# Performance work log

Measured on AMD Instinct MI355X. Metric: run time of the kernel, lower is better.

The kernel has to match this reference:

```python
import jax, jax.numpy as jnp
import numpy as np

OUT = 7            # output_size
SR = 2             # sampling_ratio (samples per bin per axis)
SCALES = (0.25, 0.125, 0.0625, 0.03125)
CANON_SIZE = 224.0
CANON_LVL = 4.0
MIN_LVL = 2
IMG = 800.0


def setup_inputs() -> dict:
    key = jax.random.key(0)
    kf = jax.random.split(key, 6)
    B, C, R = 2, 256, 256
    sizes = [200, 100, 50, 25]
    feats = [jax.random.normal(kf[i], (B, C, s, s), jnp.float32) for i, s in enumerate(sizes)]
    # valid xyxy boxes in [0, IMG], log-uniform side lengths -> spread across FPN levels
    ctr = jax.random.uniform(kf[4], (B, R, 2), minval=0.0, maxval=IMG)
    wh = jnp.exp(jax.random.uniform(kf[5], (B, R, 2), minval=float(np.log(16.0)), maxval=float(np.log(512.0))))
    lo = jnp.clip(ctr - wh / 2, 0.0, IMG)
    hi = jnp.clip(ctr + wh / 2, 0.0, IMG)
    boxes = jnp.concatenate([lo, hi], axis=-1)  # [B,R,4]
    return {"feat0": feats[0], "feat1": feats[1], "feat2": feats[2], "feat3": feats[3], "boxes": boxes}


def _prep(c, lim):
    """torchvision ROIAlign (aligned=False) bilinear index prep.
    c: sample coords [N,OUT,SR]; lim: per-box feature extent (H or W) [N]."""
    limb = lim[:, None, None]
    valid = (c > -1.0) & (c < limb)          # out-of-range samples contribute 0
    cc = jnp.maximum(c, 0.0)
    low = jnp.floor(cc)
    cap = limb - 1.0
    at_edge = low >= cap                      # y_low >= H-1 -> clamp, frac = 0
    low = jnp.minimum(low, cap)
    high = jnp.minimum(low + 1.0, cap)
    cc = jnp.where(at_edge, low, cc)
    frac = cc - low
    return valid, low.astype(jnp.int32), high.astype(jnp.int32), frac


def roi_pooler(feats, boxes):
    B, R = boxes.shape[0], boxes.shape[1]
    C = feats[0].shape[1]
    N = B * R
    flat = boxes.reshape(N, 4)
    bidx = jnp.repeat(jnp.arange(B, dtype=jnp.int32), R)  # batch index per ROI

    # level assignment (assign_boxes_to_levels)
    area = (flat[:, 2] - flat[:, 0]) * (flat[:, 3] - flat[:, 1])
    lvl = jnp.floor(CANON_LVL + jnp.log2(jnp.sqrt(area) / CANON_SIZE + 1e-8))
    lvl = jnp.clip(lvl, MIN_LVL, MIN_LVL + len(feats) - 1).astype(jnp.int32) - MIN_LVL  # [N] in [0,3]

    # pad all levels to P2 size and stack so each ROI is sampled once at its level
    Hm, Wm = feats[0].shape[2], feats[0].shape[3]
    padded = jnp.stack([jnp.pad(f, ((0, 0), (0, 0), (0, Hm - f.shape[2]), (0, Wm - f.shape[3]))) for f in feats])
    fp = padded.transpose(0, 1, 3, 4, 2)  # [L,B,Hm,Wm,C] channels-last for gather
    Hs = jnp.array([f.shape[2] for f in feats], jnp.float32)[lvl]
    Ws = jnp.array([f.shape[3] for f in feats], jnp.float32)[lvl]
    scale = jnp.array(SCALES, jnp.float32)[lvl]

    # ROIAlign aligned=False: scale coords, clamp roi size to >= 1
    x1 = flat[:, 0] * scale
    y1 = flat[:, 1] * scale
    x2 = flat[:, 2] * scale
    y2 = flat[:, 3] * scale
    roi_w = jnp.maximum(x2 - x1, 1.0)
    roi_h = jnp.maximum(y2 - y1, 1.0)
    bw = roi_w / OUT
    bh = roi_h / OUT

    # sample grid: bin index + sub-sample offsets -> [N,OUT,SR]
    grid = jnp.arange(OUT, dtype=jnp.float32)[None, :, None] + (jnp.arange(SR, dtype=jnp.float32)[None, None, :] + 0.5) / SR
    ys = y1[:, None, None] + bh[:, None, None] * grid
    xs = x1[:, None, None] + bw[:, None, None] * grid

    vy, yl, yh, fy = _prep(ys, Hs)
    vx, xl, xh, fx = _prep(xs, Ws)

    P = OUT * OUT * SR * SR  # all sample points per ROI

    def by(a):  # y-axis quantity -> broadcast over (out_y,out_x,sr_y,sr_x)
        return jnp.broadcast_to(a[:, :, None, :, None], (N, OUT, OUT, SR, SR)).reshape(N, P)

    def bx(a):
        return jnp.broadcast_to(a[:, None, :, None, :], (N, OUT, OUT, SR, SR)).reshape(N, P)

    YL, YH, FY, VY = by(yl), by(yh), by(fy), by(vy)
    XL, XH, FX, VX = bx(xl), bx(xh), bx(fx), bx(vx)

    li = lvl[:, None]
    bi = bidx[:, None]
    v00 = fp[li, bi, YL, XL]  # [N,P,C]
    v01 = fp[li, bi, YL, XH]
    v10 = fp[li, bi, YH, XL]
    v11 = fp[li, bi, YH, XH]

    w = lambda a: a[..., None]
    val = (w((1 - FY) * (1 - FX)) * v00 + w((1 - FY) * FX) * v01
           + w(FY * (1 - FX)) * v10 + w(FY * FX) * v11)
    val = val * w((VY & VX).astype(val.dtype))
    out = val.reshape(N, OUT, OUT, SR * SR, C).mean(axis=3)  # average over SR*SR samples
    return out.transpose(0, 3, 1, 2)  # [N,C,OUT,OUT]


def reference(feat0, feat1, feat2, feat3, boxes):
    return roi_pooler([feat0, feat1, feat2, feat3], boxes)
```

## Files before the change

### kernel.cpp

```cpp
#include <hip/hip_runtime.h>
#include <math.h>

typedef unsigned short u16;
typedef unsigned int   u32;

#define OUTSZ 7
#define B_ 2
#define C_ 256
#define R_ 256
#define N_ (B_ * R_)

#define PX_TOTAL 106250
#define WS_INFO_OFF 0
#define WS_NHWC_OFF (512 * 1024)
#define WS_NEEDED (WS_NHWC_OFF + (size_t)PX_TOTAL * 256 * 2)

struct RoiInfo2 {
    int pxBase, W;
    float wy0[14], wy1[14], wx0[14], wx1[14];
    short yl[14], yh[14], xl[14], xh[14];
};

__device__ __forceinline__ u16 f2bf(float v) {
    u32 u = __float_as_uint(v);
    u += 0x7fffu + ((u >> 16) & 1u);
    return (u16)(u >> 16);
}

__device__ __forceinline__ u32 pack2bf(float a, float b) {
    return (u32)f2bf(a) | ((u32)f2bf(b) << 16);
}

__global__ __launch_bounds__(256) void roi_prep(const float* __restrict__ boxes,
                                                RoiInfo2* __restrict__ info)
{
    int n = blockIdx.x * 256 + threadIdx.x;
    if (n >= N_) return;

    const float* bx = boxes + (size_t)n * 4;
    float x1 = bx[0], y1 = bx[1], x2 = bx[2], y2 = bx[3];
    float area = (x2 - x1) * (y2 - y1);
    float lf = floorf(4.0f + log2f(sqrtf(area) / 224.0f + 1e-8f));
    lf = fminf(fmaxf(lf, 2.0f), 5.0f);
    int lvl = (int)lf - 2;

    const float scales[4] = {0.25f, 0.125f, 0.0625f, 0.03125f};
    const int   sizes[4]  = {200, 100, 50, 25};
    const int   bases[4]  = {0, 80000, 100000, 105000};
    float scale = scales[lvl];
    int   HW    = sizes[lvl];
    int   b     = n >> 8;

    float fx1 = x1 * scale, fy1 = y1 * scale;
    float roi_w = fmaxf(x2 * scale - fx1, 1.0f);
    float roi_h = fmaxf(y2 * scale - fy1, 1.0f);
    float bw = roi_w / (float)OUTSZ;
    float bh = roi_h / (float)OUTSZ;

    RoiInfo2 ri;
    ri.W = HW;
    ri.pxBase = bases[lvl] + b * HW * HW;

    float lim = (float)HW, cap = lim - 1.0f;
    #pragma unroll
    for (int i = 0; i < 14; ++i) {
        float g = (float)(i >> 1) + ((float)(i & 1) + 0.5f) * 0.5f;
        {
            float c = fy1 + bh * g;
            bool  v = (c > -1.0f) && (c < lim);
            float cc = fmaxf(c, 0.0f);
            float low = floorf(cc);
            bool  edge = low >= cap;
            low = fminf(low, cap);
            float high = fminf(low + 1.0f, cap);
            float fr = edge ? 0.0f : (cc - low);
            ri.yl[i] = (short)(int)low;
            ri.yh[i] = (short)(int)high;
            ri.wy0[i] = v ? (1.0f - fr) : 0.0f;
            ri.wy1[i] = v ? fr : 0.0f;
        }
        {
            float c = fx1 + bw * g;
            bool  v = (c > -1.0f) && (c < lim);
            float cc = fmaxf(c, 0.0f);
            float low = floorf(cc);
            bool  edge = low >= cap;
            low = fminf(low, cap);
            float high = fminf(low + 1.0f, cap);
            float fr = edge ? 0.0f : (cc - low);
            ri.xl[i] = (short)(int)low;
            ri.xh[i] = (short)(int)high;
            ri.wx0[i] = v ? (1.0f - fr) : 0.0f;
            ri.wx1[i] = v ? fr : 0.0f;
        }
    }
    info[n] = ri;
}

__global__ __launch_bounds__(256) void nhwc_cast(
    const float* __restrict__ f0, const float* __restrict__ f1,
    const float* __restrict__ f2, const float* __restrict__ f3,
    u16* __restrict__ dst)
{
    __shared__ u32 lds32[256 * 32];
    const int tid  = threadIdx.x;
    const int lane = tid & 63;
    const int wave = tid >> 6;

    const int t  = blockIdx.x;
    const int cb = blockIdx.y;
    const int b  = blockIdx.z;
    const float* src; int HWsz, dstBase, ft;
    if      (t < 157) { src = f0; HWsz = 40000; dstBase = 0;      ft = t;       }
    else if (t < 197) { src = f1; HWsz = 10000; dstBase = 80000;  ft = t - 157; }
    else if (t < 207) { src = f2; HWsz = 2500;  dstBase = 100000; ft = t - 197; }
    else              { src = f3; HWsz = 625;   dstBase = 105000; ft = t - 207; }

    const int fbase = ft * 256;
    const int cw    = cb * 64 + wave * 16;
    const int rem   = HWsz - fbase;
    const int p0    = 4 * lane;
    const bool vec  = ((HWsz & 3) == 0) && (p0 + 3 < rem);

    const float* base = src + ((size_t)(b * C_ + cw)) * HWsz + fbase;

    float f[16][4];
    #pragma unroll
    for (int i = 0; i < 16; ++i) {
        const float* row = base + (size_t)i * HWsz;
        if (vec) {
            float4 v = *(const float4*)(row + p0);
            f[i][0] = v.x; f[i][1] = v.y; f[i][2] = v.z; f[i][3] = v.w;
        } else {
            #pragma unroll
            for (int k = 0; k < 4; ++k)
                f[i][k] = (p0 + k < rem) ? row[p0 + k] : 0.0f;
        }
    }

    #pragma unroll
    for (int r = 0; r < 2; ++r) {
        #pragma unroll
        for (int j = 0; j < 4; ++j) {
            uint4 o;
            o.x = pack2bf(f[r * 8 + 0][j], f[r * 8 + 1][j]);
            o.y = pack2bf(f[r * 8 + 2][j], f[r * 8 + 3][j]);
            o.z = pack2bf(f[r * 8 + 4][j], f[r * 8 + 5][j]);
            o.w = pack2bf(f[r * 8 + 6][j], f[r * 8 + 7][j]);
            const int q = (wave * 2 + r) ^ (lane & 7);
            *(uint4*)&lds32[(p0 + j) * 32 + q * 4] = o;
        }
    }
    __syncthreads();

    const int maxpx = rem < 256 ? rem : 256;
    #pragma unroll
    for (int i = 0; i < 8; ++i) {
        const int idx = i * 256 + tid;
        const int px  = idx >> 3;
        const int sub = idx & 7;
        if (px < maxpx) {
            const int q = sub ^ ((px >> 2) & 7);
            uint4 o = *(const uint4*)&lds32[px * 32 + q * 4];
            *(uint4*)(dst + (size_t)(dstBase + b * HWsz + fbase + px) * 256 + cb * 64 + sub * 8) = o;
        }
    }
}

__global__ __launch_bounds__(256) void roi_gather(
    const u16* __restrict__ ws16, const RoiInfo2* __restrict__ info,
    float* __restrict__ out)
{
    __shared__ float lds[128 * 49];
    const int g    = blockIdx.x;
    const int n    = blockIdx.y;
    const int tid  = threadIdx.x;
    const int lane = tid & 63;
    const int wave = tid >> 6;
    const RoiInfo2& ri = info[n];
    const int W = ri.W, base = ri.pxBase;
    const int c0 = g * 128;

    for (int cell = wave; cell < 49; cell += 4) {
        const int cu = __builtin_amdgcn_readfirstlane(cell);
        const int oy = cu / 7, ox = cu - oy * 7;
        float a0 = 0.0f, a1 = 0.0f;
        #pragma unroll
        for (int sy = 0; sy < 2; ++sy) {
            const int ei = oy * 2 + sy;
            const float wy0 = ri.wy0[ei], wy1 = ri.wy1[ei];
            const int rl = base + ri.yl[ei] * W;
            const int rh = base + ri.yh[ei] * W;
            #pragma unroll
            for (int sx = 0; sx < 2; ++sx) {
                const int ej = ox * 2 + sx;
                const float w00 = wy0 * ri.wx0[ej], w01 = wy0 * ri.wx1[ej];
                const float w10 = wy1 * ri.wx0[ej], w11 = wy1 * ri.wx1[ej];
                const int xl = ri.xl[ej], xh = ri.xh[ej];
                u32 u00 = ((const u32*)(ws16 + (size_t)(rl + xl) * 256 + c0))[lane];
                u32 u01 = ((const u32*)(ws16 + (size_t)(rl + xh) * 256 + c0))[lane];
                u32 u10 = ((const u32*)(ws16 + (size_t)(rh + xl) * 256 + c0))[lane];
                u32 u11 = ((const u32*)(ws16 + (size_t)(rh + xh) * 256 + c0))[lane];
                a0 += w00 * __uint_as_float(u00 << 16) + w01 * __uint_as_float(u01 << 16)
                    + w10 * __uint_as_float(u10 << 16) + w11 * __uint_as_float(u11 << 16);
                a1 += w00 * __uint_as_float(u00 & 0xffff0000u) + w01 * __uint_as_float(u01 & 0xffff0000u)
                    + w10 * __uint_as_float(u10 & 0xffff0000u) + w11 * __uint_as_float(u11 & 0xffff0000u);
            }
        }
        lds[(2 * lane) * 49 + cu]     = a0 * 0.25f;
        lds[(2 * lane + 1) * 49 + cu] = a1 * 0.25f;
    }
    __syncthreads();

    const float4* lv = (const float4*)lds;
    float4* ov = (float4*)(out + ((size_t)(n * C_ + c0)) * 49);
    for (int i = tid; i < 1568; i += 256) ov[i] = lv[i];
}

__global__ __launch_bounds__(256) void roi_direct(
    const float* __restrict__ f0, const float* __restrict__ f1,
    const float* __restrict__ f2, const float* __restrict__ f3,
    const float* __restrict__ boxes, float* __restrict__ out)
{
    const int total = B_ * R_ * C_ * OUTSZ * OUTSZ;
    int idx = blockIdx.x * blockDim.x + threadIdx.x;
    if (idx >= total) return;
    int ox = idx % 7, oy = (idx / 7) % 7, c = (idx / 49) % C_, n = idx / (49 * C_), b = n >> 8;
    const float* bx = boxes + (size_t)n * 4;
    float x1 = bx[0], y1 = bx[1], x2 = bx[2], y2 = bx[3];
    float lf = floorf(4.0f + log2f(sqrtf((x2 - x1) * (y2 - y1)) / 224.0f + 1e-8f));
    int lvl = (int)fminf(fmaxf(lf, 2.0f), 5.0f) - 2;
    const float scales[4] = {0.25f, 0.125f, 0.0625f, 0.03125f};
    const int sizes[4] = {200, 100, 50, 25};
    float scale = scales[lvl]; int HW = sizes[lvl];
    const float* fl = lvl == 0 ? f0 : lvl == 1 ? f1 : lvl == 2 ? f2 : f3;
    float fx1 = x1 * scale, fy1 = y1 * scale;
    float bw = fmaxf(x2 * scale - fx1, 1.0f) / 7.0f, bh = fmaxf(y2 * scale - fy1, 1.0f) / 7.0f;
    const float* plane = fl + ((size_t)(b * C_ + c)) * HW * HW;
    float lim = (float)HW, cap = lim - 1.0f, acc = 0.0f;
    #pragma unroll
    for (int sy = 0; sy < 2; sy++) {
        float yc = fy1 + bh * ((float)oy + ((float)sy + 0.5f) * 0.5f);
        bool vy = (yc > -1.0f) && (yc < lim);
        float ccy = fmaxf(yc, 0.0f), lowy = floorf(ccy);
        bool ey = lowy >= cap; lowy = fminf(lowy, cap);
        float highy = fminf(lowy + 1.0f, cap);
        float wfy = ey ? 0.0f : (ccy - lowy);
        int yl = (int)lowy, yh = (int)highy;
        #pragma unroll
        for (int sx = 0; sx < 2; sx++) {
            float xc = fx1 + bw * ((float)ox + ((float)sx + 0.5f) * 0.5f);
            bool vx = (xc > -1.0f) && (xc < lim);
            float ccx = fmaxf(xc, 0.0f), lowx = floorf(ccx);
            bool ex = lowx >= cap; lowx = fminf(lowx, cap);
            float highx = fminf(lowx + 1.0f, cap);
            float wfx = ex ? 0.0f : (ccx - lowx);
            int xl = (int)lowx, xh = (int)highx;
            if (vy && vx) {
                float v00 = plane[yl * HW + xl], v01 = plane[yl * HW + xh];
                float v10 = plane[yh * HW + xl], v11 = plane[yh * HW + xh];
                acc += (1.0f - wfy) * ((1.0f - wfx) * v00 + wfx * v01)
                     + wfy * ((1.0f - wfx) * v10 + wfx * v11);
            }
        }
    }
    out[idx] = acc * 0.25f;
}

extern "C" void kernel_launch(void* const* d_in, const int* in_sizes, int n_in,
                              void* d_out, int out_size, void* d_ws, size_t ws_size,
                              hipStream_t stream) {
    const float* f0    = (const float*)d_in[0];
    const float* f1    = (const float*)d_in[1];
    const float* f2    = (const float*)d_in[2];
    const float* f3    = (const float*)d_in[3];
    const float* boxes = (const float*)d_in[4];
    float* out = (float*)d_out;

    if (ws_size < WS_NEEDED) {
        const int total = B_ * R_ * C_ * OUTSZ * OUTSZ;
        roi_direct<<<(total + 255) / 256, 256, 0, stream>>>(f0, f1, f2, f3, boxes, out);
        return;
    }

    RoiInfo2* info = (RoiInfo2*)((char*)d_ws + WS_INFO_OFF);
    u16*      nhwc = (u16*)((char*)d_ws + WS_NHWC_OFF);

    roi_prep<<<dim3(2), 256, 0, stream>>>(boxes, info);
    nhwc_cast<<<dim3(210, 4, 2), 256, 0, stream>>>(f0, f1, f2, f3, nhwc);
    roi_gather<<<dim3(2, N_), 256, 0, stream>>>(nhwc, info, out);
}
```

Measured before the change: 189.7 us.

## Fold ROI prep into gather, split gather by cells, halve cast LDS

Removes the separate roi_prep kernel launch: each gather block now computes its ROI's sampling indices and weights into shared memory. The gather blocks are split over output cells instead of channels, so each lane reads 4 contiguous bf16 channels (uint2) and writes through a padded LDS tile with nontemporal stores. The nhwc_cast kernel halves its LDS footprint by staging in two passes and raises occupancy via launch bounds, and uses nontemporal loads. This trades extra per-block prep work and a scattered output store pattern for one fewer launch and higher cast occupancy.

```diff
diff --git a/kernel.cpp b/kernel.cpp
--- a/kernel.cpp
+++ b/kernel.cpp
@@ -3,6 +3,7 @@
 
 typedef unsigned short u16;
 typedef unsigned int   u32;
+typedef float f32x4 __attribute__((ext_vector_type(4)));
 
 #define OUTSZ 7
 #define B_ 2
@@ -11,15 +12,7 @@
 #define N_ (B_ * R_)
 
 #define PX_TOTAL 106250
-#define WS_INFO_OFF 0
-#define WS_NHWC_OFF (512 * 1024)
-#define WS_NEEDED (WS_NHWC_OFF + (size_t)PX_TOTAL * 256 * 2)
-
-struct RoiInfo2 {
-    int pxBase, W;
-    float wy0[14], wy1[14], wx0[14], wx1[14];
-    short yl[14], yh[14], xl[14], xh[14];
-};
+#define WS_NEEDED ((size_t)PX_TOTAL * 256 * 2)
 
 __device__ __forceinline__ u16 f2bf(float v) {
     u32 u = __float_as_uint(v);
@@ -31,78 +24,12 @@
     return (u32)f2bf(a) | ((u32)f2bf(b) << 16);
 }
 
-__global__ __launch_bounds__(256) void roi_prep(const float* __restrict__ boxes,
-                                                RoiInfo2* __restrict__ info)
-{
-    int n = blockIdx.x * 256 + threadIdx.x;
-    if (n >= N_) return;
-
-    const float* bx = boxes + (size_t)n * 4;
-    float x1 = bx[0], y1 = bx[1], x2 = bx[2], y2 = bx[3];
-    float area = (x2 - x1) * (y2 - y1);
-    float lf = floorf(4.0f + log2f(sqrtf(area) / 224.0f + 1e-8f));
-    lf = fminf(fmaxf(lf, 2.0f), 5.0f);
-    int lvl = (int)lf - 2;
-
-    const float scales[4] = {0.25f, 0.125f, 0.0625f, 0.03125f};
-    const int   sizes[4]  = {200, 100, 50, 25};
-    const int   bases[4]  = {0, 80000, 100000, 105000};
-    float scale = scales[lvl];
-    int   HW    = sizes[lvl];
-    int   b     = n >> 8;
-
-    float fx1 = x1 * scale, fy1 = y1 * scale;
-    float roi_w = fmaxf(x2 * scale - fx1, 1.0f);
-    float roi_h = fmaxf(y2 * scale - fy1, 1.0f);
-    float bw = roi_w / (float)OUTSZ;
-    float bh = roi_h / (float)OUTSZ;
-
-    RoiInfo2 ri;
-    ri.W = HW;
-    ri.pxBase = bases[lvl] + b * HW * HW;
-
-    float lim = (float)HW, cap = lim - 1.0f;
-    #pragma unroll
-    for (int i = 0; i < 14; ++i) {
-        float g = (float)(i >> 1) + ((float)(i & 1) + 0.5f) * 0.5f;
-        {
-            float c = fy1 + bh * g;
-            bool  v = (c > -1.0f) && (c < lim);
-            float cc = fmaxf(c, 0.0f);
-            float low = floorf(cc);
-            bool  edge = low >= cap;
-            low = fminf(low, cap);
-            float high = fminf(low + 1.0f, cap);
-            float fr = edge ? 0.0f : (cc - low);
-            ri.yl[i] = (short)(int)low;
-            ri.yh[i] = (short)(int)high;
-            ri.wy0[i] = v ? (1.0f - fr) : 0.0f;
-            ri.wy1[i] = v ? fr : 0.0f;
-        }
-        {
-            float c = fx1 + bw * g;
-            bool  v = (c > -1.0f) && (c < lim);
-            float cc = fmaxf(c, 0.0f);
-            float low = floorf(cc);
-            bool  edge = low >= cap;
-            low = fminf(low, cap);
-            float high = fminf(low + 1.0f, cap);
-            float fr = edge ? 0.0f : (cc - low);
-            ri.xl[i] = (short)(int)low;
-            ri.xh[i] = (short)(int)high;
-            ri.wx0[i] = v ? (1.0f - fr) : 0.0f;
-            ri.wx1[i] = v ? fr : 0.0f;
-        }
-    }
-    info[n] = ri;
-}
-
-__global__ __launch_bounds__(256) void nhwc_cast(
+__global__ __launch_bounds__(256, 8) void nhwc_cast(
     const float* __restrict__ f0, const float* __restrict__ f1,
     const float* __restrict__ f2, const float* __restrict__ f3,
     u16* __restrict__ dst)
 {
-    __shared__ u32 lds32[256 * 32];
+    __shared__ u32 lds32[128 * 32];
     const int tid  = threadIdx.x;
     const int lane = tid & 63;
     const int wave = tid >> 6;
@@ -129,7 +56,7 @@
     for (int i = 0; i < 16; ++i) {
         const float* row = base + (size_t)i * HWsz;
         if (vec) {
-            float4 v = *(const float4*)(row + p0);
+            f32x4 v = __builtin_nontemporal_load((const f32x4*)(row + p0));
             f[i][0] = v.x; f[i][1] = v.y; f[i][2] = v.z; f[i][3] = v.w;
         } else {
             #pragma unroll
@@ -138,83 +65,153 @@
         }
     }
 
+    const int half  = lane >> 5;
+    const int pl0   = p0 & 127;
+    const int maxpx = rem < 256 ? rem : 256;
+
     #pragma unroll
-    for (int r = 0; r < 2; ++r) {
+    for (int h = 0; h < 2; ++h) {
+        if (half == h) {
+            #pragma unroll
+            for (int r = 0; r < 2; ++r) {
+                #pragma unroll
+                for (int j = 0; j < 4; ++j) {
+                    uint4 o;
+                    o.x = pack2bf(f[r * 8 + 0][j], f[r * 8 + 1][j]);
+                    o.y = pack2bf(f[r * 8 + 2][j], f[r * 8 + 3][j]);
+                    o.z = pack2bf(f[r * 8 + 4][j], f[r * 8 + 5][j]);
+                    o.w = pack2bf(f[r * 8 + 6][j], f[r * 8 + 7][j]);
+                    const int q = (wave * 2 + r) ^ (lane & 7);
+                    *(uint4*)&lds32[(pl0 + j) * 32 + q * 4] = o;
+                }
+            }
+        }
+        __syncthreads();
+
         #pragma unroll
-        for (int j = 0; j < 4; ++j) {
-            uint4 o;
-            o.x = pack2bf(f[r * 8 + 0][j], f[r * 8 + 1][j]);
-            o.y = pack2bf(f[r * 8 + 2][j], f[r * 8 + 3][j]);
-            o.z = pack2bf(f[r * 8 + 4][j], f[r * 8 + 5][j]);
-            o.w = pack2bf(f[r * 8 + 6][j], f[r * 8 + 7][j]);
-            const int q = (wave * 2 + r) ^ (lane & 7);
-            *(uint4*)&lds32[(p0 + j) * 32 + q * 4] = o;
-        }
-    }
-    __syncthreads();
-
-    const int maxpx = rem < 256 ? rem : 256;
-    #pragma unroll
-    for (int i = 0; i < 8; ++i) {
-        const int idx = i * 256 + tid;
-        const int px  = idx >> 3;
-        const int sub = idx & 7;
-        if (px < maxpx) {
-            const int q = sub ^ ((px >> 2) & 7);
-            uint4 o = *(const uint4*)&lds32[px * 32 + q * 4];
-            *(uint4*)(dst + (size_t)(dstBase + b * HWsz + fbase + px) * 256 + cb * 64 + sub * 8) = o;
-        }
+        for (int i = 0; i < 4; ++i) {
+            const int idx = i * 256 + tid;
+            const int pxl = idx >> 3;
+            const int sub = idx & 7;
+            const int px  = h * 128 + pxl;
+            if (px < maxpx) {
+                const int q = sub ^ ((pxl >> 2) & 7);
+                uint4 o = *(const uint4*)&lds32[pxl * 32 + q * 4];
+                *(uint4*)(dst + (size_t)(dstBase + b * HWsz + fbase + px) * 256 + cb * 64 + sub * 8) = o;
+            }
+        }
+        if (h == 0) __syncthreads();
+    }
+}
+
+__device__ __forceinline__ void acc4(float4& a, uint2 u, float w) {
+    a.x += w * __uint_as_float(u.x << 16);
+    a.y += w * __uint_as_float(u.x & 0xffff0000u);
+    a.z += w * __uint_as_float(u.y << 16);
+    a.w += w * __uint_as_float(u.y & 0xffff0000u);
+}
+
+template<int NC, int CB>
+__device__ __forceinline__ void store_out(const float* lds, float* out, int n) {
+    #pragma unroll 4
+    for (int i = threadIdx.x; i < 256 * NC; i += 256) {
+        const int c = i / NC;
+        const int j = i - c * NC;
+        __builtin_nontemporal_store(lds[j * 260 + c],
+                                    out + ((size_t)(n * C_ + c)) * 49 + CB + j);
     }
 }
 
 __global__ __launch_bounds__(256) void roi_gather(
-    const u16* __restrict__ ws16, const RoiInfo2* __restrict__ info,
+    const u16* __restrict__ ws16, const float* __restrict__ boxes,
     float* __restrict__ out)
 {
-    __shared__ float lds[128 * 49];
+    __shared__ float lds[28 * 260];
+    __shared__ float s_wy0[14], s_wy1[14], s_wx0[14], s_wx1[14];
+    __shared__ int   s_yl[14], s_yh[14], s_xl[14], s_xh[14];
+    __shared__ int   s_base, s_W;
+
     const int g    = blockIdx.x;
     const int n    = blockIdx.y;
     const int tid  = threadIdx.x;
     const int lane = tid & 63;
     const int wave = tid >> 6;
-    const RoiInfo2& ri = info[n];
-    const int W = ri.W, base = ri.pxBase;
-    const int c0 = g * 128;
-
-    for (int cell = wave; cell < 49; cell += 4) {
+
+    if (tid < 28) {
+        const float* bx = boxes + (size_t)n * 4;
+        float x1 = bx[0], y1 = bx[1], x2 = bx[2], y2 = bx[3];
+        float area = (x2 - x1) * (y2 - y1);
+        float lf = floorf(4.0f + log2f(sqrtf(area) / 224.0f + 1e-8f));
+        lf = fminf(fmaxf(lf, 2.0f), 5.0f);
+        int lvl = (int)lf - 2;
+        const float scales[4] = {0.25f, 0.125f, 0.0625f, 0.03125f};
+        const int   sizes[4]  = {200, 100, 50, 25};
+        const int   bases[4]  = {0, 80000, 100000, 105000};
+        float scale = scales[lvl];
+        int   HW    = sizes[lvl];
+        float lim = (float)HW, cap = lim - 1.0f;
+        float fx1 = x1 * scale, fy1 = y1 * scale;
+        float bw = fmaxf(x2 * scale - fx1, 1.0f) / (float)OUTSZ;
+        float bh = fmaxf(y2 * scale - fy1, 1.0f) / (float)OUTSZ;
+        if (tid == 0) { s_base = bases[lvl] + (n >> 8) * HW * HW; s_W = HW; }
+
+        const int  i   = (tid < 14) ? tid : tid - 14;
+        const bool isy = tid < 14;
+        float o  = isy ? fy1 : fx1;
+        float st = isy ? bh  : bw;
+        float gq = (float)(i >> 1) + ((float)(i & 1) + 0.5f) * 0.5f;
+        float c = o + st * gq;
+        bool  v = (c > -1.0f) && (c < lim);
+        float cc = fmaxf(c, 0.0f);
+        float low = floorf(cc);
+        bool  edge = low >= cap;
+        low = fminf(low, cap);
+        float high = fminf(low + 1.0f, cap);
+        float fr = edge ? 0.0f : (cc - low);
+        float w0 = v ? (1.0f - fr) : 0.0f;
+        float w1 = v ? fr : 0.0f;
+        if (isy) { s_yl[i] = (int)low; s_yh[i] = (int)high; s_wy0[i] = w0; s_wy1[i] = w1; }
+        else     { s_xl[i] = (int)low; s_xh[i] = (int)high; s_wx0[i] = w0; s_wx1[i] = w1; }
+    }
+    __syncthreads();
+
+    const int base = s_base, W = s_W;
+    const int CB = g ? 28 : 0;
+    const int NC = g ? 21 : 28;
+
+    for (int cell = CB + wave; cell < CB + NC; cell += 4) {
         const int cu = __builtin_amdgcn_readfirstlane(cell);
         const int oy = cu / 7, ox = cu - oy * 7;
-        float a0 = 0.0f, a1 = 0.0f;
+        float4 acc = {0.0f, 0.0f, 0.0f, 0.0f};
         #pragma unroll
         for (int sy = 0; sy < 2; ++sy) {
             const int ei = oy * 2 + sy;
-            const float wy0 = ri.wy0[ei], wy1 = ri.wy1[ei];
-            const int rl = base + ri.yl[ei] * W;
-            const int rh = base + ri.yh[ei] * W;
+            const float wy0 = s_wy0[ei], wy1 = s_wy1[ei];
+            const int rl = base + s_yl[ei] * W;
+            const int rh = base + s_yh[ei] * W;
             #pragma unroll
             for (int sx = 0; sx < 2; ++sx) {
                 const int ej = ox * 2 + sx;
-                const float w00 = wy0 * ri.wx0[ej], w01 = wy0 * ri.wx1[ej];
-                const float w10 = wy1 * ri.wx0[ej], w11 = wy1 * ri.wx1[ej];
-                const int xl = ri.xl[ej], xh = ri.xh[ej];
-                u32 u00 = ((const u32*)(ws16 + (size_t)(rl + xl) * 256 + c0))[lane];
-                u32 u01 = ((const u32*)(ws16 + (size_t)(rl + xh) * 256 + c0))[lane];
-                u32 u10 = ((const u32*)(ws16 + (size_t)(rh + xl) * 256 + c0))[lane];
-                u32 u11 = ((const u32*)(ws16 + (size_t)(rh + xh) * 256 + c0))[lane];
-                a0 += w00 * __uint_as_float(u00 << 16) + w01 * __uint_as_float(u01 << 16)
-                    + w10 * __uint_as_float(u10 << 16) + w11 * __uint_as_float(u11 << 16);
-                a1 += w00 * __uint_as_float(u00 & 0xffff0000u) + w01 * __uint_as_float(u01 & 0xffff0000u)
-                    + w10 * __uint_as_float(u10 & 0xffff0000u) + w11 * __uint_as_float(u11 & 0xffff0000u);
-            }
-        }
-        lds[(2 * lane) * 49 + cu]     = a0 * 0.25f;
-        lds[(2 * lane + 1) * 49 + cu] = a1 * 0.25f;
+                const float w00 = wy0 * s_wx0[ej], w01 = wy0 * s_wx1[ej];
+                const float w10 = wy1 * s_wx0[ej], w11 = wy1 * s_wx1[ej];
+                const int xl = s_xl[ej], xh = s_xh[ej];
+                uint2 u00 = ((const uint2*)(ws16 + (size_t)(rl + xl) * 256))[lane];
+                uint2 u01 = ((const uint2*)(ws16 + (size_t)(rl + xh) * 256))[lane];
+                uint2 u10 = ((const uint2*)(ws16 + (size_t)(rh + xl) * 256))[lane];
+                uint2 u11 = ((const uint2*)(ws16 + (size_t)(rh + xh) * 256))[lane];
+                acc4(acc, u00, w00);
+                acc4(acc, u01, w01);
+                acc4(acc, u10, w10);
+                acc4(acc, u11, w11);
+            }
+        }
+        acc.x *= 0.25f; acc.y *= 0.25f; acc.z *= 0.25f; acc.w *= 0.25f;
+        *(float4*)&lds[(cell - CB) * 260 + 4 * lane] = acc;
     }
     __syncthreads();
 
-    const float4* lv = (const float4*)lds;
-    float4* ov = (float4*)(out + ((size_t)(n * C_ + c0)) * 49);
-    for (int i = tid; i < 1568; i += 256) ov[i] = lv[i];
+    if (g == 0) store_out<28, 0>(lds, out, n);
+    else        store_out<21, 28>(lds, out, n);
 }
 
 __global__ __launch_bounds__(256) void roi_direct(
@@ -283,10 +280,8 @@
         return;
     }
 
-    RoiInfo2* info = (RoiInfo2*)((char*)d_ws + WS_INFO_OFF);
-    u16*      nhwc = (u16*)((char*)d_ws + WS_NHWC_OFF);
-
-    roi_prep<<<dim3(2), 256, 0, stream>>>(boxes, info);
+    u16* nhwc = (u16*)d_ws;
+
     nhwc_cast<<<dim3(210, 4, 2), 256, 0, stream>>>(f0, f1, f2, f3, nhwc);
-    roi_gather<<<dim3(2, N_), 256, 0, stream>>>(nhwc, info, out);
-}
+    roi_gather<<<dim3(2, N_), 256, 0, stream>>>(nhwc, boxes, out);
+}
```

Result: slower. 205.8 us (+8.5%).
